# Kernel optimization log

Measured on AMD Instinct MI355X. Metric: run time of the kernel, lower is better.

## Reference

```python
import jax, jax.numpy as jnp
import numpy as np

B, T, D, H = 2, 2048, 1024, 16
DK = D // H


def setup_inputs() -> dict:
    key = jax.random.key(0)
    ks = jax.random.split(key, 11)
    s = 0.02
    inp = {
        "q": jax.random.normal(ks[0], (B, T, D), jnp.float32),
        "k": jax.random.normal(ks[1], (B, T, D), jnp.float32),
        "v": jax.random.normal(ks[2], (B, T, D), jnp.float32),
        # True = masked (causal), broadcast over batch and heads
        "attn_mask": jnp.triu(jnp.ones((T, T), bool), k=1)[None, None],
        "Wq": jax.random.normal(ks[3], (D, D), jnp.float32) * s,
        "bq": jnp.zeros((D,), jnp.float32),
        "Wk": jax.random.normal(ks[4], (D, D), jnp.float32) * s,
        "bk": jnp.zeros((D,), jnp.float32),
        "Wv": jax.random.normal(ks[5], (D, D), jnp.float32) * s,
        "bv": jnp.zeros((D,), jnp.float32),
        "Wo": jax.random.normal(ks[6], (D, D), jnp.float32) * s,
        "bo": jnp.zeros((D,), jnp.float32),
    }
    return inp


def _split_heads(x):
    # [B,T,D] -> [B,H,T,DK]
    return x.reshape(B, T, H, DK).transpose(0, 2, 1, 3)


def reference(q, k, v, attn_mask, Wq, bq, Wk, bk, Wv, bv, Wo, bo):
    query = _split_heads(q @ Wq.T + bq)
    key_ = _split_heads(k @ Wk.T + bk)
    value = _split_heads(v @ Wv.T + bv)
    scale = 1.0 / jnp.sqrt(jnp.asarray(DK, query.dtype))
    scores = jnp.einsum("bhqd,bhkd->bhqk", query, key_) * scale
    scores = jnp.where(attn_mask, -jnp.inf, scores)
    probs = jax.nn.softmax(scores, axis=-1)  # dropout p=0.0 (eval)
    ctx = jnp.einsum("bhqk,bhkd->bhqd", probs, value)
    ctx = ctx.transpose(0, 2, 1, 3).reshape(B, T, D)
    return ctx @ Wo.T + bo
```

## Files before the change

### kernel.cpp

```cpp
#include <hip/hip_runtime.h>
#include <stdint.h>

#define Bsz 2
#define Tseq 2048
#define Dmodel 1024
#define Hn 16
#define DKd 64

typedef __bf16 bf16;
typedef bf16 bf16x8 __attribute__((ext_vector_type(8)));
typedef float f32x4 __attribute__((ext_vector_type(4)));

__device__ inline void gld_lds16(const void* g, void* l) {
  __builtin_amdgcn_global_load_lds(
      (const __attribute__((address_space(1))) uint32_t*)g,
      (__attribute__((address_space(3))) uint32_t*)l, 16, 0, 0);
}

struct CvtArgs {
  const float* src[7];
  bf16* dst[7];
  int n4[7];
};

__global__ void __launch_bounds__(256) cvt_f32_bf16(CvtArgs a) {
  const int z = blockIdx.y;
  const float4* s = (const float4*)a.src[z];
  uint2* d = (uint2*)a.dst[z];
  const int n4 = a.n4[z];
  for (int i = blockIdx.x * 256 + threadIdx.x; i < n4; i += gridDim.x * 256) {
    float4 v = s[i];
    union { bf16 h[4]; uint2 u; } pk;
    pk.h[0] = (bf16)v.x; pk.h[1] = (bf16)v.y;
    pk.h[2] = (bf16)v.z; pk.h[3] = (bf16)v.w;
    d[i] = pk.u;
  }
}

struct GemmArgs {
  const bf16* A[3];
  const bf16* W[3];
  const float* bias[3];
  void* out[3];
  int mode[3];
  float scale[3];
};

__global__ void __launch_bounds__(256) gemm_qkv(GemmArgs g) {
  const int l = blockIdx.x;
  const int z = l >> 8;
  const int r = l & 255;
  const int mt = (r & 7) * 4 + (r >> 6);
  const int nt = (r >> 3) & 7;
  const bf16* __restrict__ A = g.A[z];
  const bf16* __restrict__ W = g.W[z];
  const float* __restrict__ bias = g.bias[z];
  const int mode = g.mode[z];
  const float scl = g.scale[z];

  __shared__ __align__(16) bf16 As[128 * 32];
  __shared__ __align__(16) bf16 Bs[128 * 32];

  const int tid = threadIdx.x;
  const int w = tid >> 6, lane = tid & 63;
  const int l15 = lane & 15, quad = lane >> 4;
  const int wm = (w >> 1) * 64, wn = (w & 1) * 64;
  const int m0 = mt * 128, n0 = nt * 128;

  f32x4 zero = {0.f, 0.f, 0.f, 0.f};
  f32x4 acc[4][4];
#pragma unroll
  for (int mi = 0; mi < 4; ++mi)
#pragma unroll
    for (int ni = 0; ni < 4; ++ni) acc[mi][ni] = zero;

  for (int k0 = 0; k0 < Dmodel; k0 += 32) {
    __syncthreads();
#pragma unroll
    for (int p = 0; p < 2; ++p) {
      const int c = p * 256 + tid;
      const int row = c >> 2, ko = (c & 3) * 8;
      gld_lds16(A + (size_t)(m0 + row) * Dmodel + k0 + ko, (void*)(As + c * 8));
      gld_lds16(W + (size_t)(n0 + row) * Dmodel + k0 + ko, (void*)(Bs + c * 8));
    }
    __syncthreads();

    bf16x8 af[4], bfr[4];
#pragma unroll
    for (int i = 0; i < 4; ++i) {
      af[i]  = *(const bf16x8*)(As + (wm + i * 16 + l15) * 32 + quad * 8);
      bfr[i] = *(const bf16x8*)(Bs + (wn + i * 16 + l15) * 32 + quad * 8);
    }
#pragma unroll
    for (int mi = 0; mi < 4; ++mi)
#pragma unroll
      for (int ni = 0; ni < 4; ++ni)
        acc[mi][ni] = __builtin_amdgcn_mfma_f32_16x16x32_bf16(af[mi], bfr[ni],
                                                              acc[mi][ni], 0, 0, 0);
  }

#pragma unroll
  for (int mi = 0; mi < 4; ++mi) {
#pragma unroll
    for (int r2 = 0; r2 < 4; ++r2) {
      const int m = m0 + wm + mi * 16 + quad * 4 + r2;
      const int bb = m >> 11, tt = m & 2047;
#pragma unroll
      for (int ni = 0; ni < 4; ++ni) {
        const int n = n0 + wn + ni * 16 + l15;
        const float val = (acc[mi][ni][r2] + bias[n]) * scl;
        bf16* o = (bf16*)g.out[z];
        const int hh = n >> 6, dk = n & 63;
        if (mode == 0) {
          o[((size_t)(bb * Hn + hh) * Tseq + tt) * DKd + dk] = (bf16)val;
        } else {
          o[((size_t)(bb * Hn + hh) * DKd + dk) * Tseq + tt] = (bf16)val;
        }
      }
    }
  }
}

__global__ void __launch_bounds__(256) gemm_out64(const bf16* __restrict__ A,
                                                  const bf16* __restrict__ W,
                                                  const float* __restrict__ bias,
                                                  float* __restrict__ out) {
  const int l = blockIdx.x;
  const int mt = (l & 7) * 8 + (l >> 6);
  const int nt = (l >> 3) & 7;

  __shared__ __align__(16) bf16 As[64 * 32];
  __shared__ __align__(16) bf16 Bs[128 * 32];

  const int tid = threadIdx.x;
  const int w = tid >> 6, lane = tid & 63;
  const int l15 = lane & 15, quad = lane >> 4;
  const int wm = (w >> 1) * 32, wn = (w & 1) * 64;
  const int m0 = mt * 64, n0 = nt * 128;

  f32x4 zero = {0.f, 0.f, 0.f, 0.f};
  f32x4 acc[2][4];
#pragma unroll
  for (int mi = 0; mi < 2; ++mi)
#pragma unroll
    for (int ni = 0; ni < 4; ++ni) acc[mi][ni] = zero;

  for (int k0 = 0; k0 < Dmodel; k0 += 32) {
    __syncthreads();
    {
      const int c = tid;
      const int row = c >> 2, ko = (c & 3) * 8;
      gld_lds16(A + (size_t)(m0 + row) * Dmodel + k0 + ko, (void*)(As + c * 8));
    }
#pragma unroll
    for (int p = 0; p < 2; ++p) {
      const int c = p * 256 + tid;
      const int row = c >> 2, ko = (c & 3) * 8;
      gld_lds16(W + (size_t)(n0 + row) * Dmodel + k0 + ko, (void*)(Bs + c * 8));
    }
    __syncthreads();

    bf16x8 af[2], bfr[4];
#pragma unroll
    for (int i = 0; i < 2; ++i)
      af[i] = *(const bf16x8*)(As + (wm + i * 16 + l15) * 32 + quad * 8);
#pragma unroll
    for (int i = 0; i < 4; ++i)
      bfr[i] = *(const bf16x8*)(Bs + (wn + i * 16 + l15) * 32 + quad * 8);
#pragma unroll
    for (int mi = 0; mi < 2; ++mi)
#pragma unroll
      for (int ni = 0; ni < 4; ++ni)
        acc[mi][ni] = __builtin_amdgcn_mfma_f32_16x16x32_bf16(af[mi], bfr[ni],
                                                              acc[mi][ni], 0, 0, 0);
  }

#pragma unroll
  for (int mi = 0; mi < 2; ++mi)
#pragma unroll
    for (int r = 0; r < 4; ++r) {
      const int m = m0 + wm + mi * 16 + quad * 4 + r;
#pragma unroll
      for (int ni = 0; ni < 4; ++ni) {
        const int n = n0 + wn + ni * 16 + l15;
        out[(size_t)m * Dmodel + n] = acc[mi][ni][r] + bias[n];
      }
    }
}

__global__ void __launch_bounds__(256) attn_fused(const bf16* __restrict__ Q,
                                                  const bf16* __restrict__ K,
                                                  const bf16* __restrict__ Vt,
                                                  bf16* __restrict__ ctx) {
  __shared__ __align__(16) bf16 Ks[8 * 128 * 8];
  __shared__ __align__(16) bf16 Vs[16 * 64 * 8];
  __shared__ __align__(16) bf16 plds[4][16][136];

  const int tid = threadIdx.x;
  const int w = tid >> 6, lane = tid & 63;
  const int l15 = lane & 15, quad = lane >> 4;

  const int l = blockIdx.x;
  const int qt = (Tseq / 64 - 1) - (l >> 5);
  const int hb = l & 31;
  const int h = hb & 15, b = hb >> 4;
  const int bh = b * Hn + h;
  const int qb = qt * 64 + w * 16;

  const bf16* Qb = Q + (size_t)bh * Tseq * DKd;
  const bf16* Kb = K + (size_t)bh * Tseq * DKd;
  const bf16* Vb = Vt + (size_t)bh * DKd * Tseq;

  bf16x8 aq0 = *(const bf16x8*)(Qb + (size_t)(qb + l15) * DKd + quad * 8);
  bf16x8 aq1 = *(const bf16x8*)(Qb + (size_t)(qb + l15) * DKd + 32 + quad * 8);

  f32x4 zero = {0.f, 0.f, 0.f, 0.f};
  f32x4 oacc[4];
#pragma unroll
  for (int nd = 0; nd < 4; ++nd) oacc[nd] = zero;
  f32x4 lacc = zero;

  bf16x8 onesf;
#pragma unroll
  for (int i = 0; i < 8; ++i) onesf[i] = (bf16)1.0f;

  const int qmax = qt * 64 + 48;
  for (int j0 = 0; j0 <= qmax; j0 += 128) {
    __syncthreads();
#pragma unroll
    for (int p = 0; p < 4; ++p) {
      const int c = p * 256 + tid;
      gld_lds16(Kb + (size_t)(j0 + (c & 127)) * DKd + (c >> 7) * 8,
                (void*)(Ks + c * 8));
      gld_lds16(Vb + (size_t)(c & 63) * Tseq + j0 + (c >> 6) * 8,
                (void*)(Vs + c * 8));
    }
    __syncthreads();

    if (j0 <= qb) {
      f32x4 s[8];
#pragma unroll
      for (int ct = 0; ct < 8; ++ct) s[ct] = zero;
#pragma unroll
      for (int ct = 0; ct < 8; ++ct) {
        bf16x8 bk0 = *(const bf16x8*)(Ks + ((quad)*128 + ct * 16 + l15) * 8);
        bf16x8 bk1 = *(const bf16x8*)(Ks + ((4 + quad) * 128 + ct * 16 + l15) * 8);
        s[ct] = __builtin_amdgcn_mfma_f32_16x16x32_bf16(aq0, bk0, s[ct], 0, 0, 0);
        s[ct] = __builtin_amdgcn_mfma_f32_16x16x32_bf16(aq1, bk1, s[ct], 0, 0, 0);
      }

      if (j0 + 128 <= qb) {
#pragma unroll
        for (int r = 0; r < 4; ++r)
#pragma unroll
          for (int ct = 0; ct < 8; ++ct)
            plds[w][quad * 4 + r][ct * 16 + l15] = (bf16)exp2f(s[ct][r]);
      } else {
#pragma unroll
        for (int r = 0; r < 4; ++r) {
          const int qrow = qb + quad * 4 + r;
#pragma unroll
          for (int ct = 0; ct < 8; ++ct) {
            const int col = j0 + ct * 16 + l15;
            const float p = exp2f(s[ct][r]);
            plds[w][quad * 4 + r][ct * 16 + l15] = (bf16)((col <= qrow) ? p : 0.f);
          }
        }
      }

      bf16x8 ap[4];
#pragma unroll
      for (int kc = 0; kc < 4; ++kc)
        ap[kc] = *(const bf16x8*)(&plds[w][l15][kc * 32 + quad * 8]);

#pragma unroll
      for (int kc = 0; kc < 4; ++kc) {
        lacc = __builtin_amdgcn_mfma_f32_16x16x32_bf16(ap[kc], onesf, lacc, 0, 0, 0);
#pragma unroll
        for (int nd = 0; nd < 4; ++nd) {
          bf16x8 bv = *(const bf16x8*)(Vs + ((kc * 4 + quad) * 64 + nd * 16 + l15) * 8);
          oacc[nd] = __builtin_amdgcn_mfma_f32_16x16x32_bf16(ap[kc], bv, oacc[nd], 0, 0, 0);
        }
      }
    }
  }

  float inv[4];
#pragma unroll
  for (int r = 0; r < 4; ++r) inv[r] = 1.0f / lacc[r];
  bf16* cb = ctx + ((size_t)(b * Tseq + qb + quad * 4)) * Dmodel + h * DKd;
#pragma unroll
  for (int nd = 0; nd < 4; ++nd)
#pragma unroll
    for (int r = 0; r < 4; ++r)
      cb[(size_t)r * Dmodel + nd * 16 + l15] = (bf16)(oacc[nd][r] * inv[r]);
}

extern "C" void kernel_launch(void* const* d_in, const int* in_sizes, int n_in,
                              void* d_out, int out_size, void* d_ws, size_t ws_size,
                              hipStream_t stream) {
  const float* q = (const float*)d_in[0];
  const float* k = (const float*)d_in[1];
  const float* v = (const float*)d_in[2];
  const float* Wq = (const float*)d_in[4];
  const float* bq = (const float*)d_in[5];
  const float* Wk = (const float*)d_in[6];
  const float* bk = (const float*)d_in[7];
  const float* Wv = (const float*)d_in[8];
  const float* bv = (const float*)d_in[9];
  const float* Wo = (const float*)d_in[10];
  const float* bo = (const float*)d_in[11];

  char* ws = (char*)d_ws;
  const size_t MB = 1024 * 1024;
  bf16* Wq_b = (bf16*)(ws + 0 * MB);
  bf16* Wk_b = (bf16*)(ws + 2 * MB);
  bf16* Wv_b = (bf16*)(ws + 4 * MB);
  bf16* Wo_b = (bf16*)(ws + 6 * MB);
  bf16* q_b  = (bf16*)(ws + 8 * MB);
  bf16* k_b  = (bf16*)(ws + 16 * MB);
  bf16* v_b  = (bf16*)(ws + 24 * MB);
  bf16* Qh   = (bf16*)(ws + 32 * MB);
  bf16* Kh   = (bf16*)(ws + 40 * MB);
  bf16* Vt   = (bf16*)(ws + 48 * MB);
  bf16* ctx  = (bf16*)(ws + 8 * MB);

  const int NACT4 = (Bsz * Tseq * Dmodel) / 4;
  const int NW4 = (Dmodel * Dmodel) / 4;

  CvtArgs ca;
  ca.src[0] = q;  ca.dst[0] = q_b;  ca.n4[0] = NACT4;
  ca.src[1] = k;  ca.dst[1] = k_b;  ca.n4[1] = NACT4;
  ca.src[2] = v;  ca.dst[2] = v_b;  ca.n4[2] = NACT4;
  ca.src[3] = Wq; ca.dst[3] = Wq_b; ca.n4[3] = NW4;
  ca.src[4] = Wk; ca.dst[4] = Wk_b; ca.n4[4] = NW4;
  ca.src[5] = Wv; ca.dst[5] = Wv_b; ca.n4[5] = NW4;
  ca.src[6] = Wo; ca.dst[6] = Wo_b; ca.n4[6] = NW4;
  cvt_f32_bf16<<<dim3(512, 7), 256, 0, stream>>>(ca);

  const float SC = 0.125f * 1.4426950408889634f;
  GemmArgs ga;
  ga.A[0] = q_b; ga.W[0] = Wq_b; ga.bias[0] = bq; ga.out[0] = Qh; ga.mode[0] = 0; ga.scale[0] = SC;
  ga.A[1] = k_b; ga.W[1] = Wk_b; ga.bias[1] = bk; ga.out[1] = Kh; ga.mode[1] = 0; ga.scale[1] = 1.f;
  ga.A[2] = v_b; ga.W[2] = Wv_b; ga.bias[2] = bv; ga.out[2] = Vt; ga.mode[2] = 1; ga.scale[2] = 1.f;
  gemm_qkv<<<dim3(768), 256, 0, stream>>>(ga);

  attn_fused<<<dim3((Tseq / 64) * Hn * Bsz), 256, 0, stream>>>(Qh, Kh, Vt, ctx);

  gemm_out64<<<dim3(512), 256, 0, stream>>>(ctx, Wo_b, bo, (float*)d_out);
}
```

Baseline: 235.2 us.

## Double attention query tile to 128 rows with transposed MFMA and diagonal skip

Each attention block now handles 128 query rows (32 per wave, two 16-row MFMA tiles) instead of 64, so every K/V tile loaded into LDS is reused by twice as many query rows. The score MFMA operands are swapped so the output is transposed, which lets exp'd probabilities and the final context be stored as packed 4-element bf16 writes. The diagonal tile computes only the key columns each wave needs. The cost is half as many blocks (512) for the GPU to spread across its compute units, more accumulator registers per thread, and per-wave imbalance on the diagonal.

```diff
diff --git a/kernel.cpp b/kernel.cpp
--- a/kernel.cpp
+++ b/kernel.cpp
@@ -15,6 +15,12 @@
   __builtin_amdgcn_global_load_lds(
       (const __attribute__((address_space(1))) uint32_t*)g,
       (__attribute__((address_space(3))) uint32_t*)l, 16, 0, 0);
+}
+
+__device__ inline void pack4_store(bf16* dst, float a, float b, float c, float d) {
+  union { bf16 h[4]; uint2 u; } pk;
+  pk.h[0] = (bf16)a; pk.h[1] = (bf16)b; pk.h[2] = (bf16)c; pk.h[3] = (bf16)d;
+  *(uint2*)dst = pk.u;
 }
 
 struct CvtArgs {
@@ -194,38 +200,39 @@
                                                   bf16* __restrict__ ctx) {
   __shared__ __align__(16) bf16 Ks[8 * 128 * 8];
   __shared__ __align__(16) bf16 Vs[16 * 64 * 8];
-  __shared__ __align__(16) bf16 plds[4][16][136];
+  __shared__ __align__(16) bf16 plds[4][32][136];
 
   const int tid = threadIdx.x;
   const int w = tid >> 6, lane = tid & 63;
   const int l15 = lane & 15, quad = lane >> 4;
 
   const int l = blockIdx.x;
-  const int qt = (Tseq / 64 - 1) - (l >> 5);
+  const int qt = 15 - (l >> 5);
   const int hb = l & 31;
   const int h = hb & 15, b = hb >> 4;
   const int bh = b * Hn + h;
-  const int qb = qt * 64 + w * 16;
+  const int qb = qt * 128 + w * 32;
 
   const bf16* Qb = Q + (size_t)bh * Tseq * DKd;
   const bf16* Kb = K + (size_t)bh * Tseq * DKd;
   const bf16* Vb = Vt + (size_t)bh * DKd * Tseq;
 
-  bf16x8 aq0 = *(const bf16x8*)(Qb + (size_t)(qb + l15) * DKd + quad * 8);
-  bf16x8 aq1 = *(const bf16x8*)(Qb + (size_t)(qb + l15) * DKd + 32 + quad * 8);
+  bf16x8 aqA0 = *(const bf16x8*)(Qb + (size_t)(qb + l15) * DKd + quad * 8);
+  bf16x8 aqA1 = *(const bf16x8*)(Qb + (size_t)(qb + l15) * DKd + 32 + quad * 8);
+  bf16x8 aqB0 = *(const bf16x8*)(Qb + (size_t)(qb + 16 + l15) * DKd + quad * 8);
+  bf16x8 aqB1 = *(const bf16x8*)(Qb + (size_t)(qb + 16 + l15) * DKd + 32 + quad * 8);
 
   f32x4 zero = {0.f, 0.f, 0.f, 0.f};
-  f32x4 oacc[4];
-#pragma unroll
-  for (int nd = 0; nd < 4; ++nd) oacc[nd] = zero;
-  f32x4 lacc = zero;
+  f32x4 oaccA[4], oaccB[4];
+#pragma unroll
+  for (int nd = 0; nd < 4; ++nd) { oaccA[nd] = zero; oaccB[nd] = zero; }
+  f32x4 laccA = zero, laccB = zero;
 
   bf16x8 onesf;
 #pragma unroll
   for (int i = 0; i < 8; ++i) onesf[i] = (bf16)1.0f;
 
-  const int qmax = qt * 64 + 48;
-  for (int j0 = 0; j0 <= qmax; j0 += 128) {
+  for (int j0 = 0; j0 <= qt * 128; j0 += 128) {
     __syncthreads();
 #pragma unroll
     for (int p = 0; p < 4; ++p) {
@@ -237,63 +244,100 @@
     }
     __syncthreads();
 
-    if (j0 <= qb) {
-      f32x4 s[8];
-#pragma unroll
-      for (int ct = 0; ct < 8; ++ct) s[ct] = zero;
+    if (j0 + 128 <= qb) {
+      f32x4 sA[8], sB[8];
+#pragma unroll
+      for (int ct = 0; ct < 8; ++ct) { sA[ct] = zero; sB[ct] = zero; }
 #pragma unroll
       for (int ct = 0; ct < 8; ++ct) {
         bf16x8 bk0 = *(const bf16x8*)(Ks + ((quad)*128 + ct * 16 + l15) * 8);
         bf16x8 bk1 = *(const bf16x8*)(Ks + ((4 + quad) * 128 + ct * 16 + l15) * 8);
-        s[ct] = __builtin_amdgcn_mfma_f32_16x16x32_bf16(aq0, bk0, s[ct], 0, 0, 0);
-        s[ct] = __builtin_amdgcn_mfma_f32_16x16x32_bf16(aq1, bk1, s[ct], 0, 0, 0);
-      }
-
-      if (j0 + 128 <= qb) {
-#pragma unroll
-        for (int r = 0; r < 4; ++r)
-#pragma unroll
-          for (int ct = 0; ct < 8; ++ct)
-            plds[w][quad * 4 + r][ct * 16 + l15] = (bf16)exp2f(s[ct][r]);
-      } else {
-#pragma unroll
-        for (int r = 0; r < 4; ++r) {
-          const int qrow = qb + quad * 4 + r;
-#pragma unroll
-          for (int ct = 0; ct < 8; ++ct) {
-            const int col = j0 + ct * 16 + l15;
-            const float p = exp2f(s[ct][r]);
-            plds[w][quad * 4 + r][ct * 16 + l15] = (bf16)((col <= qrow) ? p : 0.f);
-          }
-        }
-      }
-
-      bf16x8 ap[4];
-#pragma unroll
-      for (int kc = 0; kc < 4; ++kc)
-        ap[kc] = *(const bf16x8*)(&plds[w][l15][kc * 32 + quad * 8]);
-
+        sA[ct] = __builtin_amdgcn_mfma_f32_16x16x32_bf16(bk0, aqA0, sA[ct], 0, 0, 0);
+        sA[ct] = __builtin_amdgcn_mfma_f32_16x16x32_bf16(bk1, aqA1, sA[ct], 0, 0, 0);
+        sB[ct] = __builtin_amdgcn_mfma_f32_16x16x32_bf16(bk0, aqB0, sB[ct], 0, 0, 0);
+        sB[ct] = __builtin_amdgcn_mfma_f32_16x16x32_bf16(bk1, aqB1, sB[ct], 0, 0, 0);
+      }
+#pragma unroll
+      for (int ct = 0; ct < 8; ++ct) {
+        pack4_store(&plds[w][l15][ct * 16 + quad * 4],
+                    exp2f(sA[ct][0]), exp2f(sA[ct][1]), exp2f(sA[ct][2]), exp2f(sA[ct][3]));
+        pack4_store(&plds[w][16 + l15][ct * 16 + quad * 4],
+                    exp2f(sB[ct][0]), exp2f(sB[ct][1]), exp2f(sB[ct][2]), exp2f(sB[ct][3]));
+      }
 #pragma unroll
       for (int kc = 0; kc < 4; ++kc) {
-        lacc = __builtin_amdgcn_mfma_f32_16x16x32_bf16(ap[kc], onesf, lacc, 0, 0, 0);
+        bf16x8 bpA = *(const bf16x8*)(&plds[w][l15][kc * 32 + quad * 8]);
+        bf16x8 bpB = *(const bf16x8*)(&plds[w][16 + l15][kc * 32 + quad * 8]);
+        laccA = __builtin_amdgcn_mfma_f32_16x16x32_bf16(onesf, bpA, laccA, 0, 0, 0);
+        laccB = __builtin_amdgcn_mfma_f32_16x16x32_bf16(onesf, bpB, laccB, 0, 0, 0);
 #pragma unroll
         for (int nd = 0; nd < 4; ++nd) {
           bf16x8 bv = *(const bf16x8*)(Vs + ((kc * 4 + quad) * 64 + nd * 16 + l15) * 8);
-          oacc[nd] = __builtin_amdgcn_mfma_f32_16x16x32_bf16(ap[kc], bv, oacc[nd], 0, 0, 0);
-        }
-      }
-    }
-  }
-
-  float inv[4];
-#pragma unroll
-  for (int r = 0; r < 4; ++r) inv[r] = 1.0f / lacc[r];
-  bf16* cb = ctx + ((size_t)(b * Tseq + qb + quad * 4)) * Dmodel + h * DKd;
-#pragma unroll
-  for (int nd = 0; nd < 4; ++nd)
-#pragma unroll
-    for (int r = 0; r < 4; ++r)
-      cb[(size_t)r * Dmodel + nd * 16 + l15] = (bf16)(oacc[nd][r] * inv[r]);
+          oaccA[nd] = __builtin_amdgcn_mfma_f32_16x16x32_bf16(bv, bpA, oaccA[nd], 0, 0, 0);
+          oaccB[nd] = __builtin_amdgcn_mfma_f32_16x16x32_bf16(bv, bpB, oaccB[nd], 0, 0, 0);
+        }
+      }
+    } else {
+      const int ctfA = w * 2;
+      const int ctlA = ctfA + 1;
+      const int ctfB = w * 2 + 1;
+      const int ctlB = ctfB + 1;
+      const int kclim = w + 1;
+      for (int ct = 0; ct < ctlB; ++ct) {
+        bf16x8 bk0 = *(const bf16x8*)(Ks + ((quad)*128 + ct * 16 + l15) * 8);
+        bf16x8 bk1 = *(const bf16x8*)(Ks + ((4 + quad) * 128 + ct * 16 + l15) * 8);
+        if (ct < ctlA) {
+          f32x4 s = zero;
+          s = __builtin_amdgcn_mfma_f32_16x16x32_bf16(bk0, aqA0, s, 0, 0, 0);
+          s = __builtin_amdgcn_mfma_f32_16x16x32_bf16(bk1, aqA1, s, 0, 0, 0);
+          float p[4];
+#pragma unroll
+          for (int r = 0; r < 4; ++r) {
+            p[r] = exp2f(s[r]);
+            if (ct == ctfA && (ct * 16 + quad * 4 + r > w * 32 + l15)) p[r] = 0.f;
+          }
+          pack4_store(&plds[w][l15][ct * 16 + quad * 4], p[0], p[1], p[2], p[3]);
+        }
+        {
+          f32x4 s = zero;
+          s = __builtin_amdgcn_mfma_f32_16x16x32_bf16(bk0, aqB0, s, 0, 0, 0);
+          s = __builtin_amdgcn_mfma_f32_16x16x32_bf16(bk1, aqB1, s, 0, 0, 0);
+          float p[4];
+#pragma unroll
+          for (int r = 0; r < 4; ++r) {
+            p[r] = exp2f(s[r]);
+            if (ct == ctfB && (ct * 16 + quad * 4 + r > w * 32 + 16 + l15)) p[r] = 0.f;
+          }
+          pack4_store(&plds[w][16 + l15][ct * 16 + quad * 4], p[0], p[1], p[2], p[3]);
+        }
+      }
+      pack4_store(&plds[w][l15][ctlA * 16 + quad * 4], 0.f, 0.f, 0.f, 0.f);
+      for (int kc = 0; kc < kclim; ++kc) {
+        bf16x8 bpA = *(const bf16x8*)(&plds[w][l15][kc * 32 + quad * 8]);
+        bf16x8 bpB = *(const bf16x8*)(&plds[w][16 + l15][kc * 32 + quad * 8]);
+        laccA = __builtin_amdgcn_mfma_f32_16x16x32_bf16(onesf, bpA, laccA, 0, 0, 0);
+        laccB = __builtin_amdgcn_mfma_f32_16x16x32_bf16(onesf, bpB, laccB, 0, 0, 0);
+#pragma unroll
+        for (int nd = 0; nd < 4; ++nd) {
+          bf16x8 bv = *(const bf16x8*)(Vs + ((kc * 4 + quad) * 64 + nd * 16 + l15) * 8);
+          oaccA[nd] = __builtin_amdgcn_mfma_f32_16x16x32_bf16(bv, bpA, oaccA[nd], 0, 0, 0);
+          oaccB[nd] = __builtin_amdgcn_mfma_f32_16x16x32_bf16(bv, bpB, oaccB[nd], 0, 0, 0);
+        }
+      }
+    }
+  }
+
+  const float invA = 1.0f / laccA[0];
+  const float invB = 1.0f / laccB[0];
+  bf16* cA = ctx + (size_t)(b * Tseq + qb + l15) * Dmodel + h * DKd + quad * 4;
+  bf16* cB = ctx + (size_t)(b * Tseq + qb + 16 + l15) * Dmodel + h * DKd + quad * 4;
+#pragma unroll
+  for (int nd = 0; nd < 4; ++nd) {
+    pack4_store(cA + nd * 16, oaccA[nd][0] * invA, oaccA[nd][1] * invA,
+                oaccA[nd][2] * invA, oaccA[nd][3] * invA);
+    pack4_store(cB + nd * 16, oaccB[nd][0] * invB, oaccB[nd][1] * invB,
+                oaccB[nd][2] * invB, oaccB[nd][3] * invB);
+  }
 }
 
 extern "C" void kernel_launch(void* const* d_in, const int* in_sizes, int n_in,
@@ -345,7 +389,7 @@
   ga.A[2] = v_b; ga.W[2] = Wv_b; ga.bias[2] = bv; ga.out[2] = Vt; ga.mode[2] = 1; ga.scale[2] = 1.f;
   gemm_qkv<<<dim3(768), 256, 0, stream>>>(ga);
 
-  attn_fused<<<dim3((Tseq / 64) * Hn * Bsz), 256, 0, stream>>>(Qh, Kh, Vt, ctx);
+  attn_fused<<<dim3((Tseq / 128) * Hn * Bsz), 256, 0, stream>>>(Qh, Kh, Vt, ctx);
 
   gemm_out64<<<dim3(512), 256, 0, stream>>>(ctx, Wo_b, bo, (float*)d_out);
 }
```

Result: slower. 240.7 us (+2.3%).

## Transpose MFMA operands for packed P/ctx stores and trim diagonal-tile work

Applied to the files above, without the earlier changes.

Swaps the A/B operands of the QK^T and PV MFMAs so each lane holds four consecutive key columns (and output dims) for one query row. P can then be written to LDS, and ctx to global memory, as packed 8-byte stores instead of scattered 2-byte stores. The diagonal tile now gets its own path that computes only the 16-column subtiles up to the diagonal and only the needed PV k-chunks, zero-filling the next subtile. This cuts redundant MFMA/exp work on diagonal tiles and store instruction count. In exchange it adds a runtime-bounded loop and dynamic control flow on that path.

```diff
diff --git a/kernel.cpp b/kernel.cpp
--- a/kernel.cpp
+++ b/kernel.cpp
@@ -15,6 +15,12 @@
   __builtin_amdgcn_global_load_lds(
       (const __attribute__((address_space(1))) uint32_t*)g,
       (__attribute__((address_space(3))) uint32_t*)l, 16, 0, 0);
+}
+
+__device__ inline void pack4_store(bf16* dst, float a, float b, float c, float d) {
+  union { bf16 h[4]; uint2 u; } pk;
+  pk.h[0] = (bf16)a; pk.h[1] = (bf16)b; pk.h[2] = (bf16)c; pk.h[3] = (bf16)d;
+  *(uint2*)dst = pk.u;
 }
 
 struct CvtArgs {
@@ -237,7 +243,7 @@
     }
     __syncthreads();
 
-    if (j0 <= qb) {
+    if (j0 + 128 <= qb) {
       f32x4 s[8];
 #pragma unroll
       for (int ct = 0; ct < 8; ++ct) s[ct] = zero;
@@ -245,55 +251,61 @@
       for (int ct = 0; ct < 8; ++ct) {
         bf16x8 bk0 = *(const bf16x8*)(Ks + ((quad)*128 + ct * 16 + l15) * 8);
         bf16x8 bk1 = *(const bf16x8*)(Ks + ((4 + quad) * 128 + ct * 16 + l15) * 8);
-        s[ct] = __builtin_amdgcn_mfma_f32_16x16x32_bf16(aq0, bk0, s[ct], 0, 0, 0);
-        s[ct] = __builtin_amdgcn_mfma_f32_16x16x32_bf16(aq1, bk1, s[ct], 0, 0, 0);
-      }
-
-      if (j0 + 128 <= qb) {
-#pragma unroll
-        for (int r = 0; r < 4; ++r)
-#pragma unroll
-          for (int ct = 0; ct < 8; ++ct)
-            plds[w][quad * 4 + r][ct * 16 + l15] = (bf16)exp2f(s[ct][r]);
-      } else {
-#pragma unroll
-        for (int r = 0; r < 4; ++r) {
-          const int qrow = qb + quad * 4 + r;
-#pragma unroll
-          for (int ct = 0; ct < 8; ++ct) {
-            const int col = j0 + ct * 16 + l15;
-            const float p = exp2f(s[ct][r]);
-            plds[w][quad * 4 + r][ct * 16 + l15] = (bf16)((col <= qrow) ? p : 0.f);
-          }
-        }
-      }
-
-      bf16x8 ap[4];
-#pragma unroll
-      for (int kc = 0; kc < 4; ++kc)
-        ap[kc] = *(const bf16x8*)(&plds[w][l15][kc * 32 + quad * 8]);
-
+        s[ct] = __builtin_amdgcn_mfma_f32_16x16x32_bf16(bk0, aq0, s[ct], 0, 0, 0);
+        s[ct] = __builtin_amdgcn_mfma_f32_16x16x32_bf16(bk1, aq1, s[ct], 0, 0, 0);
+      }
+#pragma unroll
+      for (int ct = 0; ct < 8; ++ct)
+        pack4_store(&plds[w][l15][ct * 16 + quad * 4],
+                    exp2f(s[ct][0]), exp2f(s[ct][1]),
+                    exp2f(s[ct][2]), exp2f(s[ct][3]));
 #pragma unroll
       for (int kc = 0; kc < 4; ++kc) {
-        lacc = __builtin_amdgcn_mfma_f32_16x16x32_bf16(ap[kc], onesf, lacc, 0, 0, 0);
+        bf16x8 bp = *(const bf16x8*)(&plds[w][l15][kc * 32 + quad * 8]);
+        lacc = __builtin_amdgcn_mfma_f32_16x16x32_bf16(onesf, bp, lacc, 0, 0, 0);
 #pragma unroll
         for (int nd = 0; nd < 4; ++nd) {
           bf16x8 bv = *(const bf16x8*)(Vs + ((kc * 4 + quad) * 64 + nd * 16 + l15) * 8);
-          oacc[nd] = __builtin_amdgcn_mfma_f32_16x16x32_bf16(ap[kc], bv, oacc[nd], 0, 0, 0);
+          oacc[nd] = __builtin_amdgcn_mfma_f32_16x16x32_bf16(bv, bp, oacc[nd], 0, 0, 0);
         }
       }
-    }
-  }
-
-  float inv[4];
-#pragma unroll
-  for (int r = 0; r < 4; ++r) inv[r] = 1.0f / lacc[r];
-  bf16* cb = ctx + ((size_t)(b * Tseq + qb + quad * 4)) * Dmodel + h * DKd;
+    } else if (j0 <= qb) {
+      const int ctl = ((qb - j0) >> 4) + 1;
+      const int kclim = (ctl + 1) >> 1;
+      for (int ct = 0; ct < ctl; ++ct) {
+        bf16x8 bk0 = *(const bf16x8*)(Ks + ((quad)*128 + ct * 16 + l15) * 8);
+        bf16x8 bk1 = *(const bf16x8*)(Ks + ((4 + quad) * 128 + ct * 16 + l15) * 8);
+        f32x4 s = zero;
+        s = __builtin_amdgcn_mfma_f32_16x16x32_bf16(bk0, aq0, s, 0, 0, 0);
+        s = __builtin_amdgcn_mfma_f32_16x16x32_bf16(bk1, aq1, s, 0, 0, 0);
+        float p[4];
+#pragma unroll
+        for (int r = 0; r < 4; ++r) {
+          p[r] = exp2f(s[r]);
+          if (ct == ctl - 1 && (j0 + ct * 16 + quad * 4 + r > qb + l15)) p[r] = 0.f;
+        }
+        pack4_store(&plds[w][l15][ct * 16 + quad * 4], p[0], p[1], p[2], p[3]);
+      }
+      if (ctl < 8)
+        pack4_store(&plds[w][l15][ctl * 16 + quad * 4], 0.f, 0.f, 0.f, 0.f);
+      for (int kc = 0; kc < kclim; ++kc) {
+        bf16x8 bp = *(const bf16x8*)(&plds[w][l15][kc * 32 + quad * 8]);
+        lacc = __builtin_amdgcn_mfma_f32_16x16x32_bf16(onesf, bp, lacc, 0, 0, 0);
+#pragma unroll
+        for (int nd = 0; nd < 4; ++nd) {
+          bf16x8 bv = *(const bf16x8*)(Vs + ((kc * 4 + quad) * 64 + nd * 16 + l15) * 8);
+          oacc[nd] = __builtin_amdgcn_mfma_f32_16x16x32_bf16(bv, bp, oacc[nd], 0, 0, 0);
+        }
+      }
+    }
+  }
+
+  const float inv = 1.0f / lacc[0];
+  bf16* cb = ctx + (size_t)(b * Tseq + qb + l15) * Dmodel + h * DKd + quad * 4;
 #pragma unroll
   for (int nd = 0; nd < 4; ++nd)
-#pragma unroll
-    for (int r = 0; r < 4; ++r)
-      cb[(size_t)r * Dmodel + nd * 16 + l15] = (bf16)(oacc[nd][r] * inv[r]);
+    pack4_store(cb + nd * 16, oacc[nd][0] * inv, oacc[nd][1] * inv,
+                oacc[nd][2] * inv, oacc[nd][3] * inv);
 }
 
 extern "C" void kernel_launch(void* const* d_in, const int* in_sizes, int n_in,
```

After: 230.4 us. 2.1% less time.
